# Kernel optimization log

Hardware: AMD Instinct MI355X
Metric: run time of the kernel (lower is better)

The kernel has to match this reference:

```python
import jax, jax.numpy as jnp
import numpy as np

N = 100000   # nodes
E = 1600000  # edges (avg degree 16)
D = 64       # input_dim = hidden_dim = output_dim
BN_EPS = 1e-5
LEAKY_SLOPE = 0.01


def setup_inputs() -> dict:
    key = jax.random.key(0)
    ks = jax.random.split(key, 8)
    s = 1.0 / np.sqrt(D)
    return {
        "x": jax.random.normal(ks[0], (N, D), jnp.float32),
        "edge_index": jax.random.randint(ks[1], (2, E), 0, N, dtype=jnp.int32),
        "W1": jax.random.uniform(ks[2], (D, D), jnp.float32, -s, s),
        "b1": jnp.zeros((D,), jnp.float32),
        "gamma": jnp.ones((D,), jnp.float32),
        "beta": jnp.zeros((D,), jnp.float32),
        "W2": jax.random.uniform(ks[3], (D, D), jnp.float32, -s, s),
        "b2": jnp.zeros((D,), jnp.float32),
    }


def reference(x, edge_index, W1, b1, gamma, beta, W2, b2):
    n = x.shape[0]
    # GCN: add self-loops, symmetric normalization D^-1/2 (A+I) D^-1/2
    loops = jnp.arange(n, dtype=edge_index.dtype)
    src = jnp.concatenate([edge_index[0], loops])
    dst = jnp.concatenate([edge_index[1], loops])
    deg = jax.ops.segment_sum(jnp.ones_like(dst, dtype=x.dtype), dst, num_segments=n)
    dinv = jnp.where(deg > 0, jax.lax.rsqrt(jnp.maximum(deg, 1.0)), 0.0)
    norm = dinv[src] * dinv[dst]  # [E+N]

    def gcn(h, W, b):
        h = h @ W                              # [N, D]
        msg = h[src] * norm[:, None]           # gather + scale, [E+N, D]
        return jax.ops.segment_sum(msg, dst, num_segments=n) + b

    h = gcn(x, W1, b1)
    # BatchNorm1d (training-mode batch stats, biased variance)
    mu = jnp.mean(h, axis=0)
    var = jnp.mean((h - mu) ** 2, axis=0)
    h = gamma * (h - mu) * jax.lax.rsqrt(var + BN_EPS) + beta
    # LeakyReLU; dropout p=0.0 is identity
    h = jnp.where(h >= 0, h, LEAKY_SLOPE * h)
    return gcn(h, W2, b2)
```

## Files before the change

### kernel.cpp

```cpp
#include <hip/hip_runtime.h>
#include <hip/hip_fp16.h>

#define LEAKY 0.01f
#define BN_EPS 1e-5f
#define NB 256
#define NW 256
#define EMAX 7168
#define BCAP 12288

typedef int v4i __attribute__((ext_vector_type(4)));

__global__ __launch_bounds__(256) void k_part(const int* __restrict__ src,
                                              const int* __restrict__ dst,
                                              unsigned* __restrict__ barr,
                                              int* __restrict__ bofs,
                                              double* __restrict__ st,
                                              int e, int nper) {
  __shared__ int lcnt[NB], lofs[NB], lcur[NB], sd[256];
  int wb = blockIdx.x, t = threadIdx.x;
  if (wb == 0 && t < 128) st[t] = 0.0;
  int S = (e + NW - 1) / NW;
  int s0 = wb * S, s1 = min(e, s0 + S);
  lcnt[t] = 0;
  lcur[t] = 0;
  __syncthreads();
  for (int i = s0 + t; i < s1; i += 256) atomicAdd(&lcnt[dst[i] / nper], 1);
  __syncthreads();
  int v = lcnt[t];
  sd[t] = v;
  __syncthreads();
  for (int off = 1; off < 256; off <<= 1) {
    int x = (t >= off) ? sd[t - off] : 0;
    __syncthreads();
    sd[t] += x;
    __syncthreads();
  }
  lofs[t] = sd[t] - v;
  bofs[wb * (NB + 1) + t] = sd[t] - v;
  if (t == 255) bofs[wb * (NB + 1) + NB] = sd[255];
  __syncthreads();
  for (int i = s0 + t; i < s1; i += 256) {
    int d = dst[i];
    int b = d / nper;
    int r = atomicAdd(&lcur[b], 1);
    barr[s0 + lofs[b] + r] = ((unsigned)src[i] << 9) | (unsigned)(d - b * nper);
  }
}

__global__ __launch_bounds__(256) void k_mid(const unsigned* __restrict__ barr,
                                             const int* __restrict__ bofs,
                                             int* __restrict__ csr,
                                             int2* __restrict__ seg2,
                                             float* __restrict__ dinv,
                                             unsigned* __restrict__ Asent,
                                             int n, int nper, int e,
                                             const float* __restrict__ X,
                                             const float* __restrict__ W,
                                             __half* __restrict__ Y) {
  __shared__ __align__(16) int smem_i[9216];
  int t = threadIdx.x;
  if (blockIdx.x < NB) {
    int* eds    = smem_i;
    int* cnt_   = smem_i + 7168;
    int* base_  = smem_i + 7680;
    int* sd     = smem_i + 8192;
    int* ssz    = smem_i + 8448;
    int* soff   = smem_i + 8704;
    int* sstart = smem_i + 8960;
    int b = blockIdx.x;
    if (b == 0 && t < 32) Asent[t] = 0u;
    int S = (e + NW - 1) / NW;
    int lo = b * nper;
    int nn = min(nper, n - lo);
    if (nn < 0) nn = 0;
    int st_ = bofs[t * (NB + 1) + b];
    int en_ = bofs[t * (NB + 1) + b + 1];
    int v = en_ - st_;
    sstart[t] = st_;
    ssz[t] = v;
    sd[t] = v;
    __syncthreads();
    for (int off = 1; off < 256; off <<= 1) {
      int x = (t >= off) ? sd[t - off] : 0;
      __syncthreads();
      sd[t] += x;
      __syncthreads();
    }
    soff[t] = sd[t] - v;
    __syncthreads();
    int total = min(sd[255], EMAX);
    int wv = t >> 6, lane = t & 63;
    int half = lane >> 5, l32 = lane & 31;
    for (int wb = wv * 2 + half; wb < NW; wb += 8) {
      int sz = ssz[wb], of = soff[wb];
      const unsigned* rp = barr + (size_t)wb * S + sstart[wb];
      for (int k = l32; k < sz && of + k < EMAX; k += 32) eds[of + k] = (int)rp[k];
    }
    cnt_[t] = 0;
    cnt_[t + 256] = 0;
    __syncthreads();
    for (int i = t; i < total; i += 256) atomicAdd(&cnt_[eds[i] & 511], 1);
    __syncthreads();
    int c0 = cnt_[2 * t], c1 = cnt_[2 * t + 1];
    int p0 = (2 * t < nn) ? ((c0 + 15) & ~15) : 0;
    int p1 = (2 * t + 1 < nn) ? ((c1 + 15) & ~15) : 0;
    int ts = p0 + p1;
    sd[t] = ts;
    __syncthreads();
    for (int off = 1; off < 256; off <<= 1) {
      int x = (t >= off) ? sd[t - off] : 0;
      __syncthreads();
      sd[t] += x;
      __syncthreads();
    }
    int run = sd[t] - ts;
    base_[2 * t] = run;
    base_[2 * t + 1] = run + p0;
    __syncthreads();
    int bb = b * BCAP;
    for (int i = t; i < nn; i += 256) {
      int c = cnt_[i];
      int pc = (c + 15) & ~15;
      int ba = bb + base_[i];
      seg2[lo + i] = make_int2(ba, ba + pc);
      dinv[lo + i] = rsqrtf((float)(c + 1));
      for (int j = c; j < pc; j++) csr[ba + j] = n;
    }
    __syncthreads();
    cnt_[t] = 0;
    cnt_[t + 256] = 0;
    __syncthreads();
    for (int i = t; i < total; i += 256) {
      int vv = eds[i];
      int lcl = vv & 511;
      int r = atomicAdd(&cnt_[lcl], 1);
      csr[bb + base_[lcl] + r] = vv >> 9;
    }
    if (b == 0 && t == 0) dinv[n] = 0.f;
  } else {
    float(*Ws)[68] = (float(*)[68])smem_i;
    float(*Xs)[68] = (float(*)[68])(smem_i + 4352);
    int rowbase = (blockIdx.x - NB) * 64;
#pragma unroll
    for (int p = 0; p < 4; p++) {
      int idx = (p * 256 + t) * 4;
      *(float4*)&Ws[idx >> 6][idx & 63] = *(const float4*)&W[idx];
      int r = idx >> 6, c = idx & 63;
      int gr = rowbase + r;
      float4 v = (gr < n) ? *(const float4*)&X[(size_t)gr * 64 + c]
                          : make_float4(0.f, 0.f, 0.f, 0.f);
      *(float4*)&Xs[r][c] = v;
    }
    __syncthreads();
    int r = t >> 2;
    int cq = t & 3;
    float acc[16];
#pragma unroll
    for (int j = 0; j < 16; j++) acc[j] = 0.f;
#pragma unroll 4
    for (int k = 0; k < 64; k++) {
      float xv = Xs[r][k];
#pragma unroll
      for (int j = 0; j < 16; j++) acc[j] += xv * Ws[k][cq * 16 + j];
    }
    int gr = rowbase + r;
    if (gr < n) {
      __half2 h2[8];
#pragma unroll
      for (int j = 0; j < 8; j++)
        h2[j] = __floats2half2_rn(acc[2 * j], acc[2 * j + 1]);
      __half* yp = &Y[(size_t)gr * 64 + cq * 16];
      *(int4*)yp = *(int4*)&h2[0];
      *(int4*)(yp + 8) = *(int4*)&h2[4];
    }
  }
}

__global__ __launch_bounds__(256) void k_gemm2(const __half* __restrict__ Xh,
                                               const float* __restrict__ W,
                                               __half* __restrict__ Y, int n,
                                               const float* __restrict__ dinv,
                                               const double* __restrict__ st,
                                               const float* __restrict__ gamma,
                                               const float* __restrict__ beta) {
  __shared__ float Ws[64][68];
  __shared__ float Xs[64][68];
  __shared__ float smu[64], sisd[64];
  int t = threadIdx.x;
  if (t < 64) {
    double mu = st[t] / n;
    double var = st[64 + t] / n - mu * mu;
    smu[t] = (float)mu;
    sisd[t] = (float)(1.0 / sqrt(var + (double)BN_EPS));
  }
  __syncthreads();
  int rowbase = blockIdx.x * 64;
#pragma unroll
  for (int p = 0; p < 4; p++) {
    int idx = (p * 256 + t) * 4;
    *(float4*)&Ws[idx >> 6][idx & 63] = *(const float4*)&W[idx];
  }
#pragma unroll
  for (int p = 0; p < 2; p++) {
    int idx = (p * 256 + t) * 8;
    int r = idx >> 6, c = idx & 63;
    int gr = rowbase + r;
    float vp[8];
    if (gr < n) {
      int4 hv = *(const int4*)&Xh[(size_t)gr * 64 + c];
      __half2* hp = (__half2*)&hv;
#pragma unroll
      for (int q = 0; q < 4; q++) {
        float2 f = __half22float2(hp[q]);
        vp[2 * q] = f.x;
        vp[2 * q + 1] = f.y;
      }
    } else {
#pragma unroll
      for (int q = 0; q < 8; q++) vp[q] = 0.f;
    }
#pragma unroll
    for (int q = 0; q < 8; q++) {
      float z = gamma[c + q] * (vp[q] - smu[c + q]) * sisd[c + q] + beta[c + q];
      Xs[r][c + q] = (z >= 0.f) ? z : LEAKY * z;
    }
  }
  __syncthreads();
  int r = t >> 2;
  int cq = t & 3;
  float acc[16];
#pragma unroll
  for (int j = 0; j < 16; j++) acc[j] = 0.f;
#pragma unroll 4
  for (int k = 0; k < 64; k++) {
    float xv = Xs[r][k];
#pragma unroll
    for (int j = 0; j < 16; j++) acc[j] += xv * Ws[k][cq * 16 + j];
  }
  int gr = rowbase + r;
  if (gr < n) {
    float dv = dinv[gr];
    __half2 h2[8];
#pragma unroll
    for (int j = 0; j < 8; j++)
      h2[j] = __floats2half2_rn(acc[2 * j] * dv, acc[2 * j + 1] * dv);
    __half* yp = &Y[(size_t)gr * 64 + cq * 16];
    *(int4*)yp = *(int4*)&h2[0];
    *(int4*)(yp + 8) = *(int4*)&h2[4];
  }
}

template <bool WEIGHTED, bool FP16OUT>
__global__ __launch_bounds__(256) void k_agg(const __half* __restrict__ H,
                                             void* __restrict__ Optr,
                                             const int2* __restrict__ seg2,
                                             const int* __restrict__ csr,
                                             const float* __restrict__ dinv,
                                             const float* __restrict__ bias, int n) {
  int wave = (blockIdx.x * 256 + threadIdx.x) >> 6;
  int lane = threadIdx.x & 63;
  int i = wave;
  if (i >= n) return;
  float di = dinv[i];
  int2 sg = seg2[i];
  int s0 = sg.x, s1 = sg.y;
  int m = lane & 31;
  bool loA = lane < 32;
  float2 sf = __half22float2(*(const __half2*)&H[(size_t)i * 64 + 2 * m]);
  float sw = WEIGHTED ? di : 1.f;
  float a0 = loA ? sf.x * sw : 0.f;
  float a1 = loA ? sf.y * sw : 0.f;
  const v4i* cp = (const v4i*)csr;
  int j = s0 >> 2, jend = s1 >> 2;
  v4i q0 = cp[j];
  v4i q1 = cp[j + 1];
  v4i q2 = cp[j + 2];
  v4i q3 = cp[j + 3];
  for (; j < jend; j += 4) {
    v4i p0 = cp[j + 4];
    v4i p1 = cp[j + 5];
    v4i p2 = cp[j + 6];
    v4i p3 = cp[j + 7];
    int i0 = loA ? q0[0] : q0[1];
    int i1 = loA ? q0[2] : q0[3];
    int i2 = loA ? q1[0] : q1[1];
    int i3 = loA ? q1[2] : q1[3];
    int i4 = loA ? q2[0] : q2[1];
    int i5 = loA ? q2[2] : q2[3];
    int i6 = loA ? q3[0] : q3[1];
    int i7 = loA ? q3[2] : q3[3];
    float2 f0 = __half22float2(*(const __half2*)&H[(size_t)i0 * 64 + 2 * m]);
    float2 f1 = __half22float2(*(const __half2*)&H[(size_t)i1 * 64 + 2 * m]);
    float2 f2 = __half22float2(*(const __half2*)&H[(size_t)i2 * 64 + 2 * m]);
    float2 f3 = __half22float2(*(const __half2*)&H[(size_t)i3 * 64 + 2 * m]);
    float2 f4 = __half22float2(*(const __half2*)&H[(size_t)i4 * 64 + 2 * m]);
    float2 f5 = __half22float2(*(const __half2*)&H[(size_t)i5 * 64 + 2 * m]);
    float2 f6 = __half22float2(*(const __half2*)&H[(size_t)i6 * 64 + 2 * m]);
    float2 f7 = __half22float2(*(const __half2*)&H[(size_t)i7 * 64 + 2 * m]);
    if constexpr (WEIGHTED) {
      float w0 = dinv[i0], w1 = dinv[i1], w2 = dinv[i2], w3 = dinv[i3];
      float w4 = dinv[i4], w5 = dinv[i5], w6 = dinv[i6], w7 = dinv[i7];
      a0 += f0.x * w0 + f1.x * w1 + f2.x * w2 + f3.x * w3;
      a1 += f0.y * w0 + f1.y * w1 + f2.y * w2 + f3.y * w3;
      a0 += f4.x * w4 + f5.x * w5 + f6.x * w6 + f7.x * w7;
      a1 += f4.y * w4 + f5.y * w5 + f6.y * w6 + f7.y * w7;
    } else {
      a0 += f0.x + f1.x + f2.x + f3.x;
      a1 += f0.y + f1.y + f2.y + f3.y;
      a0 += f4.x + f5.x + f6.x + f7.x;
      a1 += f4.y + f5.y + f6.y + f7.y;
    }
    q0 = p0;
    q1 = p1;
    q2 = p2;
    q3 = p3;
  }
  a0 += __shfl_xor(a0, 32, 64);
  a1 += __shfl_xor(a1, 32, 64);
  if (loA) {
    float2 bv = *(const float2*)&bias[2 * m];
    float o0 = di * a0 + bv.x;
    float o1 = di * a1 + bv.y;
    if constexpr (FP16OUT) {
      ((__half2*)Optr)[(size_t)i * 32 + m] = __floats2half2_rn(o0, o1);
    } else {
      float2 o;
      o.x = o0;
      o.y = o1;
      *(float2*)&((float*)Optr)[(size_t)i * 64 + 2 * m] = o;
    }
  }
}

__global__ __launch_bounds__(256) void k_bnstats(const __half* __restrict__ H,
                                                 double* __restrict__ st, int n) {
  __shared__ double ds0[8][32], ds1[8][32], dq0[8][32], dq1[8][32];
  int t = threadIdx.x;
  int m = t & 31;
  int g = t >> 5;
  double s0 = 0.0, s1 = 0.0, q0 = 0.0, q1 = 0.0;
  const __half2* H2 = (const __half2*)H;
  for (int r = blockIdx.x * 8 + g; r < n; r += gridDim.x * 8) {
    float2 f = __half22float2(H2[(size_t)r * 32 + m]);
    s0 += f.x;
    s1 += f.y;
    q0 += (double)f.x * f.x;
    q1 += (double)f.y * f.y;
  }
  ds0[g][m] = s0;
  ds1[g][m] = s1;
  dq0[g][m] = q0;
  dq1[g][m] = q1;
  __syncthreads();
  if (g == 0) {
    double a0 = 0, a1 = 0, b0 = 0, b1 = 0;
#pragma unroll
    for (int j = 0; j < 8; j++) {
      a0 += ds0[j][m];
      a1 += ds1[j][m];
      b0 += dq0[j][m];
      b1 += dq1[j][m];
    }
    atomicAdd(&st[2 * m], a0);
    atomicAdd(&st[2 * m + 1], a1);
    atomicAdd(&st[64 + 2 * m], b0);
    atomicAdd(&st[64 + 2 * m + 1], b1);
  }
}

extern "C" void kernel_launch(void* const* d_in, const int* in_sizes, int n_in,
                              void* d_out, int out_size, void* d_ws, size_t ws_size,
                              hipStream_t stream) {
  const float* x     = (const float*)d_in[0];
  const int*   ei    = (const int*)d_in[1];
  const float* W1    = (const float*)d_in[2];
  const float* b1    = (const float*)d_in[3];
  const float* gamma = (const float*)d_in[4];
  const float* beta  = (const float*)d_in[5];
  const float* W2    = (const float*)d_in[6];
  const float* b2    = (const float*)d_in[7];
  float* out = (float*)d_out;

  int n = in_sizes[0] / 64;
  int e = in_sizes[1] / 2;
  const int* srcv = ei;
  const int* dstv = ei + e;
  int nper = (n + NB - 1) / NB;

  char* ws = (char*)d_ws;
  size_t p = 0;
  auto alloc = [&](size_t bytes) {
    void* r = ws + p;
    p += (bytes + 255) & ~(size_t)255;
    return r;
  };
  unsigned* barr = (unsigned*)alloc((size_t)(e + 256) * 4);
  int*      bofs = (int*)alloc((size_t)NW * (NB + 1) * 4);
  int*      csr  = (int*)alloc(((size_t)NB * BCAP + 256) * 4);
  int2*     seg2 = (int2*)alloc((size_t)n * 8);
  float*    dinv = (float*)alloc((size_t)(n + 1) * 4);
  double*   st   = (double*)alloc(128 * 8);
  __half*   A    = (__half*)alloc((size_t)(n + 1) * 64 * 2);
  __half*   B    = (__half*)alloc((size_t)n * 64 * 2);

  int gG = (n + 63) / 64;
  int gAgg = (n + 3) / 4;

  k_part<<<NW, 256, 0, stream>>>(srcv, dstv, barr, bofs, st, e, nper);
  k_mid<<<NB + gG, 256, 0, stream>>>(barr, bofs, csr, seg2, dinv,
                                     (unsigned*)(A + (size_t)n * 64), n, nper, e,
                                     x, W1, A);
  k_agg<true, true><<<gAgg, 256, 0, stream>>>(A, B, seg2, csr, dinv, b1, n);
  k_bnstats<<<256, 256, 0, stream>>>(B, st, n);
  k_gemm2<<<gG, 256, 0, stream>>>(B, W2, A, n, dinv, st, gamma, beta);
  k_agg<false, false><<<gAgg, 256, 0, stream>>>(A, out, seg2, csr, dinv, b2, n);
}
```

Measured before the change: 190.2 us.

## Split CSR build into 512 smaller buckets and overlap GEMM1 with partitioning

```diff
diff --git a/kernel.cpp b/kernel.cpp
--- a/kernel.cpp
+++ b/kernel.cpp
@@ -3,82 +3,43 @@
 
 #define LEAKY 0.01f
 #define BN_EPS 1e-5f
-#define NB 256
+#define NB 512
 #define NW 256
-#define EMAX 7168
-#define BCAP 12288
+#define EMAX 4096
+#define BCAP 7168
 
 typedef int v4i __attribute__((ext_vector_type(4)));
 
-__global__ __launch_bounds__(256) void k_part(const int* __restrict__ src,
-                                              const int* __restrict__ dst,
-                                              unsigned* __restrict__ barr,
-                                              int* __restrict__ bofs,
-                                              double* __restrict__ st,
-                                              int e, int nper) {
-  __shared__ int lcnt[NB], lofs[NB], lcur[NB], sd[256];
-  int wb = blockIdx.x, t = threadIdx.x;
-  if (wb == 0 && t < 128) st[t] = 0.0;
-  int S = (e + NW - 1) / NW;
-  int s0 = wb * S, s1 = min(e, s0 + S);
-  lcnt[t] = 0;
-  lcur[t] = 0;
-  __syncthreads();
-  for (int i = s0 + t; i < s1; i += 256) atomicAdd(&lcnt[dst[i] / nper], 1);
-  __syncthreads();
-  int v = lcnt[t];
-  sd[t] = v;
-  __syncthreads();
-  for (int off = 1; off < 256; off <<= 1) {
-    int x = (t >= off) ? sd[t - off] : 0;
-    __syncthreads();
-    sd[t] += x;
-    __syncthreads();
-  }
-  lofs[t] = sd[t] - v;
-  bofs[wb * (NB + 1) + t] = sd[t] - v;
-  if (t == 255) bofs[wb * (NB + 1) + NB] = sd[255];
-  __syncthreads();
-  for (int i = s0 + t; i < s1; i += 256) {
-    int d = dst[i];
-    int b = d / nper;
-    int r = atomicAdd(&lcur[b], 1);
-    barr[s0 + lofs[b] + r] = ((unsigned)src[i] << 9) | (unsigned)(d - b * nper);
-  }
-}
-
-__global__ __launch_bounds__(256) void k_mid(const unsigned* __restrict__ barr,
-                                             const int* __restrict__ bofs,
-                                             int* __restrict__ csr,
-                                             int2* __restrict__ seg2,
-                                             float* __restrict__ dinv,
-                                             unsigned* __restrict__ Asent,
-                                             int n, int nper, int e,
-                                             const float* __restrict__ X,
-                                             const float* __restrict__ W,
-                                             __half* __restrict__ Y) {
+__global__ __launch_bounds__(256) void k_pg(const int* __restrict__ src,
+                                            const int* __restrict__ dst,
+                                            unsigned* __restrict__ barr,
+                                            int* __restrict__ bofs,
+                                            double* __restrict__ st,
+                                            int e, int nper, int n,
+                                            const float* __restrict__ X,
+                                            const float* __restrict__ W,
+                                            __half* __restrict__ Y) {
   __shared__ __align__(16) int smem_i[9216];
   int t = threadIdx.x;
-  if (blockIdx.x < NB) {
-    int* eds    = smem_i;
-    int* cnt_   = smem_i + 7168;
-    int* base_  = smem_i + 7680;
-    int* sd     = smem_i + 8192;
-    int* ssz    = smem_i + 8448;
-    int* soff   = smem_i + 8704;
-    int* sstart = smem_i + 8960;
-    int b = blockIdx.x;
-    if (b == 0 && t < 32) Asent[t] = 0u;
+  if (blockIdx.x < NW) {
+    int* lcnt = smem_i;
+    int* lofs = smem_i + 512;
+    int* lcur = smem_i + 1024;
+    int* sd   = smem_i + 1536;
+    int wb = blockIdx.x;
+    if (wb == 0 && t < 128) st[t] = 0.0;
     int S = (e + NW - 1) / NW;
-    int lo = b * nper;
-    int nn = min(nper, n - lo);
-    if (nn < 0) nn = 0;
-    int st_ = bofs[t * (NB + 1) + b];
-    int en_ = bofs[t * (NB + 1) + b + 1];
-    int v = en_ - st_;
-    sstart[t] = st_;
-    ssz[t] = v;
-    sd[t] = v;
+    int s0 = wb * S, s1 = min(e, s0 + S);
+    lcnt[t] = 0;
+    lcnt[t + 256] = 0;
+    lcur[t] = 0;
+    lcur[t + 256] = 0;
+    __syncthreads();
+    for (int i = s0 + t; i < s1; i += 256) atomicAdd(&lcnt[dst[i] / nper], 1);
+    __syncthreads();
+    int c0 = lcnt[2 * t], c1 = lcnt[2 * t + 1];
+    int ts = c0 + c1;
+    sd[t] = ts;
     __syncthreads();
     for (int off = 1; off < 256; off <<= 1) {
       int x = (t >= off) ? sd[t - off] : 0;
@@ -86,61 +47,23 @@
       sd[t] += x;
       __syncthreads();
     }
-    soff[t] = sd[t] - v;
-    __syncthreads();
-    int total = min(sd[255], EMAX);
-    int wv = t >> 6, lane = t & 63;
-    int half = lane >> 5, l32 = lane & 31;
-    for (int wb = wv * 2 + half; wb < NW; wb += 8) {
-      int sz = ssz[wb], of = soff[wb];
-      const unsigned* rp = barr + (size_t)wb * S + sstart[wb];
-      for (int k = l32; k < sz && of + k < EMAX; k += 32) eds[of + k] = (int)rp[k];
-    }
-    cnt_[t] = 0;
-    cnt_[t + 256] = 0;
-    __syncthreads();
-    for (int i = t; i < total; i += 256) atomicAdd(&cnt_[eds[i] & 511], 1);
-    __syncthreads();
-    int c0 = cnt_[2 * t], c1 = cnt_[2 * t + 1];
-    int p0 = (2 * t < nn) ? ((c0 + 15) & ~15) : 0;
-    int p1 = (2 * t + 1 < nn) ? ((c1 + 15) & ~15) : 0;
-    int ts = p0 + p1;
-    sd[t] = ts;
-    __syncthreads();
-    for (int off = 1; off < 256; off <<= 1) {
-      int x = (t >= off) ? sd[t - off] : 0;
-      __syncthreads();
-      sd[t] += x;
-      __syncthreads();
-    }
     int run = sd[t] - ts;
-    base_[2 * t] = run;
-    base_[2 * t + 1] = run + p0;
-    __syncthreads();
-    int bb = b * BCAP;
-    for (int i = t; i < nn; i += 256) {
-      int c = cnt_[i];
-      int pc = (c + 15) & ~15;
-      int ba = bb + base_[i];
-      seg2[lo + i] = make_int2(ba, ba + pc);
-      dinv[lo + i] = rsqrtf((float)(c + 1));
-      for (int j = c; j < pc; j++) csr[ba + j] = n;
-    }
-    __syncthreads();
-    cnt_[t] = 0;
-    cnt_[t + 256] = 0;
-    __syncthreads();
-    for (int i = t; i < total; i += 256) {
-      int vv = eds[i];
-      int lcl = vv & 511;
-      int r = atomicAdd(&cnt_[lcl], 1);
-      csr[bb + base_[lcl] + r] = vv >> 9;
-    }
-    if (b == 0 && t == 0) dinv[n] = 0.f;
+    lofs[2 * t] = run;
+    lofs[2 * t + 1] = run + c0;
+    bofs[wb * (NB + 1) + 2 * t] = run;
+    bofs[wb * (NB + 1) + 2 * t + 1] = run + c0;
+    if (t == 255) bofs[wb * (NB + 1) + NB] = sd[255];
+    __syncthreads();
+    for (int i = s0 + t; i < s1; i += 256) {
+      int d = dst[i];
+      int b = d / nper;
+      int r = atomicAdd(&lcur[b], 1);
+      barr[s0 + lofs[b] + r] = ((unsigned)src[i] << 9) | (unsigned)(d - b * nper);
+    }
   } else {
     float(*Ws)[68] = (float(*)[68])smem_i;
     float(*Xs)[68] = (float(*)[68])(smem_i + 4352);
-    int rowbase = (blockIdx.x - NB) * 64;
+    int rowbase = (blockIdx.x - NW) * 64;
 #pragma unroll
     for (int p = 0; p < 4; p++) {
       int idx = (p * 256 + t) * 4;
@@ -167,13 +90,85 @@
     if (gr < n) {
       __half2 h2[8];
 #pragma unroll
-      for (int j = 0; j < 8; j++)
-        h2[j] = __floats2half2_rn(acc[2 * j], acc[2 * j + 1]);
+      for (int j = 0; j < 8; j++) h2[j] = __floats2half2_rn(acc[2 * j], acc[2 * j + 1]);
       __half* yp = &Y[(size_t)gr * 64 + cq * 16];
       *(int4*)yp = *(int4*)&h2[0];
       *(int4*)(yp + 8) = *(int4*)&h2[4];
     }
   }
+}
+
+__global__ __launch_bounds__(256) void k_csrb(const unsigned* __restrict__ barr,
+                                              const int* __restrict__ bofs,
+                                              int* __restrict__ csr,
+                                              int2* __restrict__ seg2,
+                                              float* __restrict__ dinv,
+                                              unsigned* __restrict__ Asent,
+                                              int n, int nper, int e) {
+  __shared__ int eds[EMAX];
+  __shared__ int cnt_[256], base_[256], sd[256];
+  __shared__ int ssz[256], soff[256], sstart[256];
+  int b = blockIdx.x, t = threadIdx.x;
+  if (b == 0 && t < 32) Asent[t] = 0u;
+  int S = (e + NW - 1) / NW;
+  int lo = b * nper;
+  int nn = min(nper, n - lo);
+  if (nn < 0) nn = 0;
+  int st_ = bofs[t * (NB + 1) + b];
+  int en_ = bofs[t * (NB + 1) + b + 1];
+  int v = en_ - st_;
+  sstart[t] = st_;
+  ssz[t] = v;
+  sd[t] = v;
+  __syncthreads();
+  for (int off = 1; off < 256; off <<= 1) {
+    int x = (t >= off) ? sd[t - off] : 0;
+    __syncthreads();
+    sd[t] += x;
+    __syncthreads();
+  }
+  soff[t] = sd[t] - v;
+  __syncthreads();
+  int total = min(sd[255], EMAX);
+  int g8 = t >> 3, l8 = t & 7;
+  for (int wb = g8; wb < NW; wb += 32) {
+    int sz = ssz[wb], of = soff[wb];
+    const unsigned* rp = barr + (size_t)wb * S + sstart[wb];
+    for (int k = l8; k < sz && of + k < EMAX; k += 8) eds[of + k] = (int)rp[k];
+  }
+  cnt_[t] = 0;
+  __syncthreads();
+  for (int i = t; i < total; i += 256) atomicAdd(&cnt_[eds[i] & 511], 1);
+  __syncthreads();
+  int c = cnt_[t];
+  int pc = (t < nn) ? ((c + 15) & ~15) : 0;
+  sd[t] = pc;
+  __syncthreads();
+  for (int off = 1; off < 256; off <<= 1) {
+    int x = (t >= off) ? sd[t - off] : 0;
+    __syncthreads();
+    sd[t] += x;
+    __syncthreads();
+  }
+  base_[t] = sd[t] - pc;
+  __syncthreads();
+  int bb = b * BCAP;
+  if (t < nn) {
+    int ba = bb + base_[t];
+    seg2[lo + t] = make_int2(ba, ba + pc);
+    dinv[lo + t] = rsqrtf((float)(c + 1));
+    for (int j = c; j < pc; j++) csr[ba + j] = n;
+  }
+  __syncthreads();
+  cnt_[t] = 0;
+  __syncthreads();
+  for (int i = t; i < total; i += 256) {
+    int vv = eds[i];
+    int lcl = vv & 511;
+    int r = atomicAdd(&cnt_[lcl], 1);
+    csr[bb + base_[lcl] + r] = vv >> 9;
+  }
+  if (b == 0 && t == 0) dinv[n] = 0.f;
 }
 
 __global__ __launch_bounds__(256) void k_gemm2(const __half* __restrict__ Xh,
@@ -406,10 +401,9 @@
   int gG = (n + 63) / 64;
   int gAgg = (n + 3) / 4;
 
-  k_part<<<NW, 256, 0, stream>>>(srcv, dstv, barr, bofs, st, e, nper);
-  k_mid<<<NB + gG, 256, 0, stream>>>(barr, bofs, csr, seg2, dinv,
-                                     (unsigned*)(A + (size_t)n * 64), n, nper, e,
-                                     x, W1, A);
+  k_pg<<<NW + gG, 256, 0, stream>>>(srcv, dstv, barr, bofs, st, e, nper, n, x, W1, A);
+  k_csrb<<<NB, 256, 0, stream>>>(barr, bofs, csr, seg2, dinv,
+                                 (unsigned*)(A + (size_t)n * 64), n, nper, e);
   k_agg<true, true><<<gAgg, 256, 0, stream>>>(A, B, seg2, csr, dinv, b1, n);
   k_bnstats<<<256, 256, 0, stream>>>(B, st, n);
   k_gemm2<<<gG, 256, 0, stream>>>(B, W2, A, n, dinv, st, gamma, beta);
```

Result: faster. 184.2 us (-3.1%).
